# Kernel tuning notes

Hardware: AMD Instinct MI355X
Metric: run time of the kernel (lower is better)

## Reference

```python
import jax, jax.numpy as jnp
import numpy as np

NH = 16
NKV = 4
ROPE_BASE = 10000.0
ROPE_TSL = 1024
EPS = 1.1920928955078125e-07  # torch fp32 finfo eps (F.rms_norm default)


def _rms_norm(t):
    return t * jax.lax.rsqrt(jnp.mean(t * t, axis=-1, keepdims=True) + EPS)


def _rope_tables(T, hd):
    # Rotary with rd = hd (rope_dims=0 -> full-head rope). NTK rescale if T > tsl.
    rd = hd
    if T > ROPE_TSL:
        base = ROPE_BASE * (T / ROPE_TSL) ** (rd / (rd - 2))
    else:
        base = ROPE_BASE
    inv_freq = 1.0 / base ** (np.arange(0, rd, 2, dtype=np.float32) / rd)
    t = np.arange(T, dtype=np.float32)
    fr = np.outer(t, inv_freq)  # [T, hd//2]
    return jnp.asarray(np.cos(fr)), jnp.asarray(np.sin(fr))


def _apply_rope(x, cos, sin):
    # x: [B,T,H,D]; cos/sin: [T, D//2] broadcast over batch & heads
    h = x.shape[-1] // 2
    x1, x2 = x[..., :h], x[..., h:]
    c = cos[None, :, None, :]
    s = sin[None, :, None, :]
    return jnp.concatenate((x1 * c + x2 * s, -x1 * s + x2 * c), axis=-1)


def setup_inputs() -> dict:
    key = jax.random.key(0)
    k1, k2, k3, k4, k5 = jax.random.split(key, 5)
    B, T, dim = 2, 2048, 2048
    hd = dim // NH
    kd = NKV * hd
    std = 0.02
    return {
        "x": jax.random.normal(k1, (B, T, dim), dtype=jnp.float32),
        "Wq": jax.random.normal(k2, (dim, dim), dtype=jnp.float32) * std,
        "Wk": jax.random.normal(k3, (kd, dim), dtype=jnp.float32) * std,
        "Wv": jax.random.normal(k4, (kd, dim), dtype=jnp.float32) * std,
        "Wp": jax.random.normal(k5, (dim, dim), dtype=jnp.float32) * std,
        "q_gain": jnp.full((NH,), 1.5, dtype=jnp.float32),
    }


def reference(x, Wq, Wk, Wv, Wp, q_gain):
    B, T, d = x.shape
    hd = d // NH
    g = NH // NKV
    q = (x @ Wq.T).reshape(B, T, NH, hd)
    k = (x @ Wk.T).reshape(B, T, NKV, hd)
    v = (x @ Wv.T).reshape(B, T, NKV, hd)
    q = _rms_norm(q)
    k = _rms_norm(k)
    cos, sin = _rope_tables(T, hd)
    q = _apply_rope(q, cos, sin)
    k = _apply_rope(k, cos, sin)
    q = q * q_gain[None, None, :, None]
    # GQA causal SDPA: group queries per kv head
    qg = q.reshape(B, T, NKV, g, hd)
    scores = jnp.einsum("btkgd,bskd->bkgts", qg, k) / jnp.sqrt(jnp.asarray(hd, x.dtype))
    causal = jnp.tril(jnp.ones((T, T), dtype=bool))
    scores = jnp.where(causal[None, None, None, :, :], scores, jnp.asarray(-jnp.inf, scores.dtype))
    attn = jax.nn.softmax(scores, axis=-1)
    y = jnp.einsum("bkgts,bskd->btkgd", attn, v).reshape(B, T, d)
    return y @ Wp.T
```

## Files before the change

### kernel.cpp

```cpp
#include <hip/hip_runtime.h>
#include <math.h>

#define NH 16
#define NKV 4
#define HD 128
#define DIM 2048
#define GQ 4
#define EPS 1.1920928955078125e-07f

typedef unsigned short u16;
using bf16x8 = __attribute__((ext_vector_type(8))) short;
using f16x4  = __attribute__((ext_vector_type(4))) _Float16;
using f32x4  = __attribute__((ext_vector_type(4))) float;

__device__ inline float fast_exp2(float x) { return __builtin_amdgcn_exp2f(x); }

__device__ inline short f2bf(float f) {
    unsigned u = __builtin_bit_cast(unsigned, f);
    return (short)((u + 0x7FFFu + ((u >> 16) & 1u)) >> 16);
}
__device__ inline u16 f2h(float f) {
    _Float16 h = (_Float16)f;
    return __builtin_bit_cast(u16, h);
}

#define ASYNC_LOAD16(g, l)                                                        \
    __builtin_amdgcn_global_load_lds(                                             \
        (const __attribute__((address_space(1))) unsigned*)(g),                   \
        (__attribute__((address_space(3))) unsigned*)(l), 16, 0, 0)

__global__ __launch_bounds__(256) void cvt_bf16(const float* __restrict__ src,
                                                u16* __restrict__ dst, int n4) {
    int i = blockIdx.x * 256 + threadIdx.x;
    if (i < n4) {
        float4 f = ((const float4*)src)[i];
        ushort4 o;
        o.x = (u16)f2bf(f.x); o.y = (u16)f2bf(f.y);
        o.z = (u16)f2bf(f.z); o.w = (u16)f2bf(f.w);
        ((ushort4*)dst)[i] = o;
    }
}

__global__ __launch_bounds__(64) void rope_tab(float* __restrict__ ct,
                                               float* __restrict__ st,
                                               double base) {
    const int t = blockIdx.x;
    const int j = threadIdx.x;
    const float inv_freq = (float)pow(base, -(double)j / 64.0);
    const float fr = (float)t * inv_freq;
    ct[t * 64 + j] = cosf(fr);
    st[t * 64 + j] = sinf(fr);
}

#define BM 256
#define BN 256
#define BKT 64
#define NKT (DIM / BKT)

template <int EPI>
__global__ __launch_bounds__(512, 2) void gemm256(
    const u16* __restrict__ A, const u16* __restrict__ W,
    float* __restrict__ C, int N,
    u16* __restrict__ q16, u16* __restrict__ k16,
    u16* __restrict__ vt16,
    const float* __restrict__ ctab, const float* __restrict__ stab,
    const float* __restrict__ q_gain, int T) {
    __shared__ u16 As[2][BM * BKT];
    __shared__ u16 Bs[2][BN * BKT];

    const int tid  = threadIdx.x;
    const int wid  = tid >> 6;
    const int lane = tid & 63;
    const int l16  = lane & 15;
    const int quad = lane >> 4;
    const int wm   = wid >> 1;
    const int wn   = wid & 1;
    const int m0   = blockIdx.x * BM;
    const int n0   = blockIdx.y * BN;
    const int K    = DIM;

    const int srow = lane >> 3;
    const int scol = ((lane & 7) ^ srow) * 8;
    const u16* pa = A + (size_t)(m0 + srow) * K + scol;
    const u16* pw = W + (size_t)(n0 + srow) * K + scol;

    const int ca0 = ((quad)     ^ (l16 & 7)) * 8;
    const int ca1 = ((4 + quad) ^ (l16 & 7)) * 8;

    f32x4 acc[4][8];
#pragma unroll
    for (int i = 0; i < 4; i++)
#pragma unroll
        for (int j = 0; j < 8; j++) acc[i][j] = (f32x4){0.f, 0.f, 0.f, 0.f};

#pragma unroll
    for (int r = 0; r < 4; r++) {
        ASYNC_LOAD16(pa + (size_t)(r * 64 + wid * 8) * K, &As[0][(r * 64 + wid * 8) * BKT]);
        ASYNC_LOAD16(pw + (size_t)(r * 64 + wid * 8) * K, &Bs[0][(r * 64 + wid * 8) * BKT]);
    }
    __syncthreads();

#pragma unroll 1
    for (int kt = 0; kt < NKT; kt++) {
        const int cur = kt & 1;
        const u16* Ac = &As[cur][0];
        const u16* Bc = &Bs[cur][0];
        u16* An = &As[cur ^ 1][0];
        u16* Bn = &Bs[cur ^ 1][0];
        const bool pf = (kt + 1 < NKT);
        const size_t ko = (size_t)(kt + 1) * BKT;

        bf16x8 a0[4], a1[4];

        {
            bf16x8 bf[4];
#pragma unroll
            for (int mt = 0; mt < 4; mt++)
                a0[mt] = *(const bf16x8*)&Ac[(wm * 64 + mt * 16 + l16) * BKT + ca0];
#pragma unroll
            for (int nt = 0; nt < 4; nt++)
                bf[nt] = *(const bf16x8*)&Bc[(wn * 128 + nt * 16 + l16) * BKT + ca0];
            if (pf) {
                ASYNC_LOAD16(pa + (size_t)(0 * 64 + wid * 8) * K + ko, &An[(0 * 64 + wid * 8) * BKT]);
                ASYNC_LOAD16(pa + (size_t)(1 * 64 + wid * 8) * K + ko, &An[(1 * 64 + wid * 8) * BKT]);
            }
            __builtin_amdgcn_sched_barrier(0);
            __builtin_amdgcn_s_barrier();
            asm volatile("s_waitcnt lgkmcnt(0)" ::: "memory");
            __builtin_amdgcn_sched_barrier(0);
            __builtin_amdgcn_s_setprio(1);
#pragma unroll
            for (int mt = 0; mt < 4; mt++)
#pragma unroll
                for (int nt = 0; nt < 4; nt++)
                    acc[mt][nt] = __builtin_amdgcn_mfma_f32_16x16x32_bf16(
                        a0[mt], bf[nt], acc[mt][nt], 0, 0, 0);
            __builtin_amdgcn_s_setprio(0);
            __builtin_amdgcn_sched_barrier(0);
            __builtin_amdgcn_s_barrier();
        }

        {
            bf16x8 bf[4];
#pragma unroll
            for (int mt = 0; mt < 4; mt++)
                a1[mt] = *(const bf16x8*)&Ac[(wm * 64 + mt * 16 + l16) * BKT + ca1];
#pragma unroll
            for (int nt = 0; nt < 4; nt++)
                bf[nt] = *(const bf16x8*)&Bc[(wn * 128 + nt * 16 + l16) * BKT + ca1];
            if (pf) {
                ASYNC_LOAD16(pa + (size_t)(2 * 64 + wid * 8) * K + ko, &An[(2 * 64 + wid * 8) * BKT]);
                ASYNC_LOAD16(pa + (size_t)(3 * 64 + wid * 8) * K + ko, &An[(3 * 64 + wid * 8) * BKT]);
            }
            __builtin_amdgcn_sched_barrier(0);
            __builtin_amdgcn_s_barrier();
            asm volatile("s_waitcnt lgkmcnt(0)" ::: "memory");
            __builtin_amdgcn_sched_barrier(0);
            __builtin_amdgcn_s_setprio(1);
#pragma unroll
            for (int mt = 0; mt < 4; mt++)
#pragma unroll
                for (int nt = 0; nt < 4; nt++)
                    acc[mt][nt] = __builtin_amdgcn_mfma_f32_16x16x32_bf16(
                        a1[mt], bf[nt], acc[mt][nt], 0, 0, 0);
            __builtin_amdgcn_s_setprio(0);
            __builtin_amdgcn_sched_barrier(0);
            __builtin_amdgcn_s_barrier();
        }

        {
            bf16x8 bf[4];
#pragma unroll
            for (int nt = 0; nt < 4; nt++)
                bf[nt] = *(const bf16x8*)&Bc[(wn * 128 + (nt + 4) * 16 + l16) * BKT + ca0];
            if (pf) {
                ASYNC_LOAD16(pw + (size_t)(0 * 64 + wid * 8) * K + ko, &Bn[(0 * 64 + wid * 8) * BKT]);
                ASYNC_LOAD16(pw + (size_t)(1 * 64 + wid * 8) * K + ko, &Bn[(1 * 64 + wid * 8) * BKT]);
            }
            __builtin_amdgcn_sched_barrier(0);
            __builtin_amdgcn_s_barrier();
            asm volatile("s_waitcnt lgkmcnt(0)" ::: "memory");
            __builtin_amdgcn_sched_barrier(0);
            __builtin_amdgcn_s_setprio(1);
#pragma unroll
            for (int mt = 0; mt < 4; mt++)
#pragma unroll
                for (int nt = 0; nt < 4; nt++)
                    acc[mt][nt + 4] = __builtin_amdgcn_mfma_f32_16x16x32_bf16(
                        a0[mt], bf[nt], acc[mt][nt + 4], 0, 0, 0);
            __builtin_amdgcn_s_setprio(0);
            __builtin_amdgcn_sched_barrier(0);
            __builtin_amdgcn_s_barrier();
        }

        {
            bf16x8 bf[4];
#pragma unroll
            for (int nt = 0; nt < 4; nt++)
                bf[nt] = *(const bf16x8*)&Bc[(wn * 128 + (nt + 4) * 16 + l16) * BKT + ca1];
            if (pf) {
                ASYNC_LOAD16(pw + (size_t)(2 * 64 + wid * 8) * K + ko, &Bn[(2 * 64 + wid * 8) * BKT]);
                ASYNC_LOAD16(pw + (size_t)(3 * 64 + wid * 8) * K + ko, &Bn[(3 * 64 + wid * 8) * BKT]);
            }
            __builtin_amdgcn_sched_barrier(0);
            __builtin_amdgcn_s_barrier();
            asm volatile("s_waitcnt lgkmcnt(0)" ::: "memory");
            __builtin_amdgcn_sched_barrier(0);
            __builtin_amdgcn_s_setprio(1);
#pragma unroll
            for (int mt = 0; mt < 4; mt++)
#pragma unroll
                for (int nt = 0; nt < 4; nt++)
                    acc[mt][nt + 4] = __builtin_amdgcn_mfma_f32_16x16x32_bf16(
                        a1[mt], bf[nt], acc[mt][nt + 4], 0, 0, 0);
            __builtin_amdgcn_s_setprio(0);
        }

        __syncthreads();
    }

    if constexpr (EPI == 0) {
#pragma unroll
        for (int mt = 0; mt < 4; mt++)
#pragma unroll
            for (int nt = 0; nt < 8; nt++)
#pragma unroll
                for (int r = 0; r < 4; r++)
                    C[(size_t)(m0 + wm * 64 + mt * 16 + quad * 4 + r) * N +
                      n0 + wn * 128 + nt * 16 + l16] = acc[mt][nt][r];
    } else {
        const int nb = n0 + wn * 128;
        if (nb < 2560) {
            const bool isQ = (nb < 2048);
            const float gval =
                isQ ? (q_gain[nb >> 7] * 0.08838834764831843f * 1.4426950408889634f)
                    : 1.0f;
#pragma unroll
            for (int mt = 0; mt < 4; mt++) {
#pragma unroll
                for (int r = 0; r < 4; r++) {
                    float s = 0.f;
#pragma unroll
                    for (int nt = 0; nt < 8; nt++) {
                        float a = acc[mt][nt][r];
                        s = fmaf(a, a, s);
                    }
                    s += __shfl_xor(s, 1);
                    s += __shfl_xor(s, 2);
                    s += __shfl_xor(s, 4);
                    s += __shfl_xor(s, 8);
                    const float scale = rsqrtf(s * (1.0f / HD) + EPS) * gval;
                    const int m = m0 + wm * 64 + mt * 16 + quad * 4 + r;
                    const int t = m & (T - 1);
                    const float* ct = ctab + t * 64;
                    const float* st = stab + t * 64;
                    u16* dst = isQ ? (q16 + (size_t)m * 2048 + nb)
                                   : (k16 + (size_t)m * 512 + (nb - 2048));
#pragma unroll
                    for (int nt = 0; nt < 4; nt++) {
                        const int j = nt * 16 + l16;
                        const float c = ct[j], sn = st[j];
                        const float x1 = acc[mt][nt][r] * scale;
                        const float x2 = acc[mt][nt + 4][r] * scale;
                        dst[j]      = (u16)f2bf(x1 * c + x2 * sn);
                        dst[j + 64] = (u16)f2bf(x2 * c - x1 * sn);
                    }
                }
            }
        } else {
#pragma unroll
            for (int mt = 0; mt < 4; mt++) {
                const int mb = m0 + wm * 64 + mt * 16 + quad * 4;
                const int b = mb >> 11;
                const int t0 = mb & (T - 1);
#pragma unroll
                for (int nt = 0; nt < 8; nt++) {
                    const int dcol = nb - 2560 + nt * 16 + l16;
                    const int kvh = dcol >> 7;
                    const int d = dcol & (HD - 1);
                    ushort4 o;
                    o.x = f2h(acc[mt][nt][0]);
                    o.y = f2h(acc[mt][nt][1]);
                    o.z = f2h(acc[mt][nt][2]);
                    o.w = f2h(acc[mt][nt][3]);
                    *(ushort4*)(vt16 + ((size_t)((b * NKV + kvh) * HD + d)) * T + t0) = o;
                }
            }
        }
    }
}

#define QT 64
#define SK 64

__global__ __launch_bounds__(256) void flash4(const u16* __restrict__ q16,
                                              const u16* __restrict__ k16,
                                              const u16* __restrict__ vt16,
                                              u16* __restrict__ y16, int T) {
    __shared__ u16 Ks[2][SK * 128];
    __shared__ u16 Vt[2][HD * 64];

    const int tid = threadIdx.x;
    const int wave = tid >> 6;
    const int lane = tid & 63;
    const int l16 = lane & 15;
    const int quad = lane >> 4;

    const int bid = blockIdx.x;
    const int bh = bid & 31;
    const int pr = bid >> 5;
    const int h = bh & 15;
    const int b = bh >> 4;
    const int kv = h / GQ;

    const u16* kg = k16 + ((size_t)b * T * NKV + kv) * HD;
    const u16* vg = vt16 + (size_t)(b * NKV + kv) * HD * T;

    const int krow_in_seg = lane >> 4;
    const int kclog_base = lane & 15;
    const int vrow_in_seg = lane >> 3;
    const int vclog = (lane & 7) ^ (lane >> 3);

#pragma unroll 1
    for (int half = 0; half < 2; half++) {
        const int qt = half ? (T / QT - 1 - pr) : pr;
        const int q0 = qt * QT;
        const int qglob = q0 + wave * 16 + l16;
        const int nts = q0 / SK + 1;

        bf16x8 qf[4];
        {
            const u16* qp = q16 + ((size_t)(b * T + qglob) * NH + h) * HD;
#pragma unroll
            for (int kc = 0; kc < 4; kc++)
                qf[kc] = *(const bf16x8*)(qp + kc * 32 + quad * 8);
        }

        f32x4 of[8];
#pragma unroll
        for (int i = 0; i < 8; i++) of[i] = (f32x4){0.f, 0.f, 0.f, 0.f};
        float m_i = -1e30f, l_i = 0.0f;

        __syncthreads();
#pragma unroll
        for (int j = 0; j < 4; j++) {
            const int seg = wave * 4 + j;
            const int r = seg * 4 + krow_in_seg;
            const int clog = kclog_base ^ (r & 15);
            ASYNC_LOAD16(kg + (size_t)r * (NKV * HD) + clog * 8, &Ks[0][seg * 512]);
            const int d = seg * 8 + vrow_in_seg;
            ASYNC_LOAD16(vg + (size_t)d * T + vclog * 8, &Vt[0][seg * 512]);
        }

        for (int it = 0; it < nts; it++) {
            const int cur = it & 1;
            __syncthreads();

            if (it + 1 < nts) {
                const int s1 = (it + 1) * SK;
#pragma unroll
                for (int j = 0; j < 4; j++) {
                    const int seg = wave * 4 + j;
                    const int r = seg * 4 + krow_in_seg;
                    const int clog = kclog_base ^ (r & 15);
                    ASYNC_LOAD16(kg + (size_t)(s1 + r) * (NKV * HD) + clog * 8,
                                 &Ks[cur ^ 1][seg * 512]);
                    const int d = seg * 8 + vrow_in_seg;
                    ASYNC_LOAD16(vg + (size_t)d * T + s1 + vclog * 8,
                                 &Vt[cur ^ 1][seg * 512]);
                }
            }

            f32x4 sf[4];
#pragma unroll
            for (int st = 0; st < 4; st++) sf[st] = (f32x4){0.f, 0.f, 0.f, 0.f};
#pragma unroll
            for (int kc = 0; kc < 4; kc++)
#pragma unroll
                for (int st = 0; st < 4; st++) {
                    const int row = st * 16 + l16;
                    bf16x8 kf = *(const bf16x8*)
                        &Ks[cur][row * 128 + (((kc * 4 + quad) ^ l16) * 8)];
                    sf[st] = __builtin_amdgcn_mfma_f32_16x16x32_bf16(kf, qf[kc], sf[st], 0, 0, 0);
                }

            if (it == nts - 1) {
#pragma unroll
                for (int st = 0; st < 4; st++)
#pragma unroll
                    for (int r = 0; r < 4; r++)
                        if (q0 + st * 16 + quad * 4 + r > qglob) sf[st][r] = -1e30f;
            }

            float tm = -1e30f;
#pragma unroll
            for (int st = 0; st < 4; st++)
#pragma unroll
                for (int r = 0; r < 4; r++) tm = fmaxf(tm, sf[st][r]);
            tm = fmaxf(tm, __shfl_xor(tm, 16));
            tm = fmaxf(tm, __shfl_xor(tm, 32));

            const float mprev = m_i;
            const float mnew = fmaxf(mprev, tm);
            m_i = mnew;
            const float alpha = fast_exp2(mprev - mnew);

            f16x4 pf[4];
            float ls = 0.0f;
#pragma unroll
            for (int st = 0; st < 4; st++)
#pragma unroll
                for (int r = 0; r < 4; r++) {
                    float e = fast_exp2(sf[st][r] - mnew);
                    ls += e;
                    pf[st][r] = (_Float16)e;
                }
            ls += __shfl_xor(ls, 16);
            ls += __shfl_xor(ls, 32);
            l_i = alpha * l_i + ls;

            if (__ballot(mnew > mprev)) {
#pragma unroll
                for (int dt = 0; dt < 8; dt++)
#pragma unroll
                    for (int r = 0; r < 4; r++) of[dt][r] *= alpha;
            }

#pragma unroll
            for (int st = 0; st < 4; st++) {
                const int clog = st * 2 + (quad >> 1);
#pragma unroll
                for (int dt = 0; dt < 8; dt++) {
                    const int d = dt * 16 + l16;
                    const int phys = clog ^ (l16 & 7);
                    f16x4 va = *(const f16x4*)
                        &Vt[cur][d * 64 + phys * 8 + (quad & 1) * 4];
                    of[dt] = __builtin_amdgcn_mfma_f32_16x16x16f16(va, pf[st], of[dt], 0, 0, 0);
                }
            }
        }

        const float inv = 1.0f / l_i;
        u16* yp = y16 + ((size_t)(b * T + qglob) * NH + h) * HD + quad * 4;
#pragma unroll
        for (int dt = 0; dt < 8; dt++) {
            ushort4 o;
            o.x = (u16)f2bf(of[dt][0] * inv);
            o.y = (u16)f2bf(of[dt][1] * inv);
            o.z = (u16)f2bf(of[dt][2] * inv);
            o.w = (u16)f2bf(of[dt][3] * inv);
            *(ushort4*)(yp + dt * 16) = o;
        }
    }
}

extern "C" void kernel_launch(void* const* d_in, const int* in_sizes, int n_in,
                              void* d_out, int out_size, void* d_ws, size_t ws_size,
                              hipStream_t stream) {
    const float* x      = (const float*)d_in[0];
    const float* Wq     = (const float*)d_in[1];
    const float* Wk     = (const float*)d_in[2];
    const float* Wv     = (const float*)d_in[3];
    const float* Wp     = (const float*)d_in[4];
    const float* q_gain = (const float*)d_in[5];
    float* out = (float*)d_out;

    const int B = 2;
    const int BT = in_sizes[0] / DIM;
    const int T = BT / B;
    const int KD = NKV * HD;

    u16* x16   = (u16*)d_ws;
    u16* wqkv  = x16 + (size_t)BT * DIM;
    u16* wp16  = wqkv + (size_t)3072 * DIM;
    u16* q16   = wp16 + (size_t)DIM * DIM;
    u16* k16   = q16 + (size_t)BT * DIM;
    u16* vt16  = k16 + (size_t)BT * KD;
    float* ctab = (float*)(vt16 + (size_t)BT * KD);
    float* stab = ctab + (size_t)T * 64;
    u16* y16   = x16;

    double base = 10000.0;
    if (T > 1024) base = 10000.0 * pow((double)T / 1024.0, 128.0 / 126.0);

    const int nx4  = BT * DIM / 4;
    const int nwq4 = DIM * DIM / 4;
    const int nwk4 = KD * DIM / 4;

    cvt_bf16<<<(nx4 + 255) / 256, 256, 0, stream>>>(x, x16, nx4);
    cvt_bf16<<<(nwq4 + 255) / 256, 256, 0, stream>>>(Wq, wqkv, nwq4);
    cvt_bf16<<<(nwk4 + 255) / 256, 256, 0, stream>>>(Wk, wqkv + (size_t)2048 * DIM, nwk4);
    cvt_bf16<<<(nwk4 + 255) / 256, 256, 0, stream>>>(Wv, wqkv + (size_t)2560 * DIM, nwk4);
    cvt_bf16<<<(nwq4 + 255) / 256, 256, 0, stream>>>(Wp, wp16, nwq4);
    rope_tab<<<T, 64, 0, stream>>>(ctab, stab, base);

    gemm256<1><<<dim3(BT / BM, 3072 / BN), 512, 0, stream>>>(
        x16, wqkv, nullptr, 0, q16, k16, vt16, ctab, stab, q_gain, T);

    flash4<<<32 * (T / QT / 2), 256, 0, stream>>>(q16, k16, vt16, y16, T);

    gemm256<0><<<dim3(BT / BM, DIM / BN), 512, 0, stream>>>(
        y16, wp16, out, DIM, nullptr, nullptr, nullptr, nullptr, nullptr, nullptr, T);
}
```

Before: 318.5 us.

## Replace full syncthreads with split vmcnt waits in GEMM prefetch pipeline

Reorders the GEMM's async global-to-LDS prefetches so that all A rows are issued first and the B halves are interleaved (rows 0/2 then 1/3). The per-iteration __syncthreads is replaced with partial s_waitcnt vmcnt waits plus raw s_barriers, so only the needed half of the next tile must have landed before its consumption phase. Prefetch is made unconditional by wrapping the k offset (extra redundant loads on the last iteration, drained by a final vmcnt(0)). It relies on exact vmcnt counting being correct; miscounted waits would race. The output-projection launch grid is rewritten as DIM/128/2, which appears equivalent to DIM/BN if BN is 256.

```diff
diff --git a/kernel.cpp b/kernel.cpp
--- a/kernel.cpp
+++ b/kernel.cpp
@@ -28,6 +28,10 @@
     __builtin_amdgcn_global_load_lds(                                             \
         (const __attribute__((address_space(1))) unsigned*)(g),                   \
         (__attribute__((address_space(3))) unsigned*)(l), 16, 0, 0)
+
+#define SCHED_FENCE() __builtin_amdgcn_sched_barrier(0)
+#define WAIT_LGKM0()  asm volatile("s_waitcnt lgkmcnt(0)" ::: "memory")
+#define WAIT_VM(N)    asm volatile("s_waitcnt vmcnt(" #N ")" ::: "memory")
 
 __global__ __launch_bounds__(256) void cvt_bf16(const float* __restrict__ src,
                                                 u16* __restrict__ dst, int n4) {
@@ -94,11 +98,16 @@
         for (int j = 0; j < 8; j++) acc[i][j] = (f32x4){0.f, 0.f, 0.f, 0.f};
 
 #pragma unroll
-    for (int r = 0; r < 4; r++) {
+    for (int r = 0; r < 4; r++)
         ASYNC_LOAD16(pa + (size_t)(r * 64 + wid * 8) * K, &As[0][(r * 64 + wid * 8) * BKT]);
-        ASYNC_LOAD16(pw + (size_t)(r * 64 + wid * 8) * K, &Bs[0][(r * 64 + wid * 8) * BKT]);
-    }
-    __syncthreads();
+    ASYNC_LOAD16(pw + (size_t)(0 * 64 + wid * 8) * K, &Bs[0][(0 * 64 + wid * 8) * BKT]);
+    ASYNC_LOAD16(pw + (size_t)(2 * 64 + wid * 8) * K, &Bs[0][(2 * 64 + wid * 8) * BKT]);
+    ASYNC_LOAD16(pw + (size_t)(1 * 64 + wid * 8) * K, &Bs[0][(1 * 64 + wid * 8) * BKT]);
+    ASYNC_LOAD16(pw + (size_t)(3 * 64 + wid * 8) * K, &Bs[0][(3 * 64 + wid * 8) * BKT]);
+    WAIT_VM(2);
+    SCHED_FENCE();
+    __builtin_amdgcn_s_barrier();
+    SCHED_FENCE();
 
 #pragma unroll 1
     for (int kt = 0; kt < NKT; kt++) {
@@ -107,8 +116,7 @@
         const u16* Bc = &Bs[cur][0];
         u16* An = &As[cur ^ 1][0];
         u16* Bn = &Bs[cur ^ 1][0];
-        const bool pf = (kt + 1 < NKT);
-        const size_t ko = (size_t)(kt + 1) * BKT;
+        const size_t ko = (size_t)((kt + 1) & (NKT - 1)) * BKT;
 
         bf16x8 a0[4], a1[4];
 
@@ -120,14 +128,14 @@
 #pragma unroll
             for (int nt = 0; nt < 4; nt++)
                 bf[nt] = *(const bf16x8*)&Bc[(wn * 128 + nt * 16 + l16) * BKT + ca0];
-            if (pf) {
-                ASYNC_LOAD16(pa + (size_t)(0 * 64 + wid * 8) * K + ko, &An[(0 * 64 + wid * 8) * BKT]);
-                ASYNC_LOAD16(pa + (size_t)(1 * 64 + wid * 8) * K + ko, &An[(1 * 64 + wid * 8) * BKT]);
-            }
-            __builtin_amdgcn_sched_barrier(0);
-            __builtin_amdgcn_s_barrier();
-            asm volatile("s_waitcnt lgkmcnt(0)" ::: "memory");
-            __builtin_amdgcn_sched_barrier(0);
+#pragma unroll
+            for (int r = 0; r < 4; r++)
+                ASYNC_LOAD16(pa + (size_t)(r * 64 + wid * 8) * K + ko,
+                             &An[(r * 64 + wid * 8) * BKT]);
+            SCHED_FENCE();
+            __builtin_amdgcn_s_barrier();
+            WAIT_LGKM0();
+            SCHED_FENCE();
             __builtin_amdgcn_s_setprio(1);
 #pragma unroll
             for (int mt = 0; mt < 4; mt++)
@@ -136,7 +144,7 @@
                     acc[mt][nt] = __builtin_amdgcn_mfma_f32_16x16x32_bf16(
                         a0[mt], bf[nt], acc[mt][nt], 0, 0, 0);
             __builtin_amdgcn_s_setprio(0);
-            __builtin_amdgcn_sched_barrier(0);
+            SCHED_FENCE();
             __builtin_amdgcn_s_barrier();
         }
 
@@ -148,14 +156,14 @@
 #pragma unroll
             for (int nt = 0; nt < 4; nt++)
                 bf[nt] = *(const bf16x8*)&Bc[(wn * 128 + nt * 16 + l16) * BKT + ca1];
-            if (pf) {
-                ASYNC_LOAD16(pa + (size_t)(2 * 64 + wid * 8) * K + ko, &An[(2 * 64 + wid * 8) * BKT]);
-                ASYNC_LOAD16(pa + (size_t)(3 * 64 + wid * 8) * K + ko, &An[(3 * 64 + wid * 8) * BKT]);
-            }
-            __builtin_amdgcn_sched_barrier(0);
-            __builtin_amdgcn_s_barrier();
-            asm volatile("s_waitcnt lgkmcnt(0)" ::: "memory");
-            __builtin_amdgcn_sched_barrier(0);
+            ASYNC_LOAD16(pw + (size_t)(0 * 64 + wid * 8) * K + ko,
+                         &Bn[(0 * 64 + wid * 8) * BKT]);
+            ASYNC_LOAD16(pw + (size_t)(2 * 64 + wid * 8) * K + ko,
+                         &Bn[(2 * 64 + wid * 8) * BKT]);
+            SCHED_FENCE();
+            __builtin_amdgcn_s_barrier();
+            WAIT_LGKM0();
+            SCHED_FENCE();
             __builtin_amdgcn_s_setprio(1);
 #pragma unroll
             for (int mt = 0; mt < 4; mt++)
@@ -164,8 +172,10 @@
                     acc[mt][nt] = __builtin_amdgcn_mfma_f32_16x16x32_bf16(
                         a1[mt], bf[nt], acc[mt][nt], 0, 0, 0);
             __builtin_amdgcn_s_setprio(0);
-            __builtin_amdgcn_sched_barrier(0);
-            __builtin_amdgcn_s_barrier();
+            WAIT_VM(6);
+            SCHED_FENCE();
+            __builtin_amdgcn_s_barrier();
+            SCHED_FENCE();
         }
 
         {
@@ -173,14 +183,14 @@
 #pragma unroll
             for (int nt = 0; nt < 4; nt++)
                 bf[nt] = *(const bf16x8*)&Bc[(wn * 128 + (nt + 4) * 16 + l16) * BKT + ca0];
-            if (pf) {
-                ASYNC_LOAD16(pw + (size_t)(0 * 64 + wid * 8) * K + ko, &Bn[(0 * 64 + wid * 8) * BKT]);
-                ASYNC_LOAD16(pw + (size_t)(1 * 64 + wid * 8) * K + ko, &Bn[(1 * 64 + wid * 8) * BKT]);
-            }
-            __builtin_amdgcn_sched_barrier(0);
-            __builtin_amdgcn_s_barrier();
-            asm volatile("s_waitcnt lgkmcnt(0)" ::: "memory");
-            __builtin_amdgcn_sched_barrier(0);
+            ASYNC_LOAD16(pw + (size_t)(1 * 64 + wid * 8) * K + ko,
+                         &Bn[(1 * 64 + wid * 8) * BKT]);
+            ASYNC_LOAD16(pw + (size_t)(3 * 64 + wid * 8) * K + ko,
+                         &Bn[(3 * 64 + wid * 8) * BKT]);
+            SCHED_FENCE();
+            __builtin_amdgcn_s_barrier();
+            WAIT_LGKM0();
+            SCHED_FENCE();
             __builtin_amdgcn_s_setprio(1);
 #pragma unroll
             for (int mt = 0; mt < 4; mt++)
@@ -189,7 +199,7 @@
                     acc[mt][nt + 4] = __builtin_amdgcn_mfma_f32_16x16x32_bf16(
                         a0[mt], bf[nt], acc[mt][nt + 4], 0, 0, 0);
             __builtin_amdgcn_s_setprio(0);
-            __builtin_amdgcn_sched_barrier(0);
+            SCHED_FENCE();
             __builtin_amdgcn_s_barrier();
         }
 
@@ -198,14 +208,10 @@
 #pragma unroll
             for (int nt = 0; nt < 4; nt++)
                 bf[nt] = *(const bf16x8*)&Bc[(wn * 128 + (nt + 4) * 16 + l16) * BKT + ca1];
-            if (pf) {
-                ASYNC_LOAD16(pw + (size_t)(2 * 64 + wid * 8) * K + ko, &Bn[(2 * 64 + wid * 8) * BKT]);
-                ASYNC_LOAD16(pw + (size_t)(3 * 64 + wid * 8) * K + ko, &Bn[(3 * 64 + wid * 8) * BKT]);
-            }
-            __builtin_amdgcn_sched_barrier(0);
-            __builtin_amdgcn_s_barrier();
-            asm volatile("s_waitcnt lgkmcnt(0)" ::: "memory");
-            __builtin_amdgcn_sched_barrier(0);
+            SCHED_FENCE();
+            __builtin_amdgcn_s_barrier();
+            WAIT_LGKM0();
+            SCHED_FENCE();
             __builtin_amdgcn_s_setprio(1);
 #pragma unroll
             for (int mt = 0; mt < 4; mt++)
@@ -214,10 +220,13 @@
                     acc[mt][nt + 4] = __builtin_amdgcn_mfma_f32_16x16x32_bf16(
                         a1[mt], bf[nt], acc[mt][nt + 4], 0, 0, 0);
             __builtin_amdgcn_s_setprio(0);
-        }
-
-        __syncthreads();
+            WAIT_VM(2);
+            SCHED_FENCE();
+            __builtin_amdgcn_s_barrier();
+            SCHED_FENCE();
+        }
     }
+    WAIT_VM(0);
 
     if constexpr (EPI == 0) {
 #pragma unroll
@@ -499,6 +508,6 @@
 
     flash4<<<32 * (T / QT / 2), 256, 0, stream>>>(q16, k16, vt16, y16, T);
 
-    gemm256<0><<<dim3(BT / BM, DIM / BN), 512, 0, stream>>>(
+    gemm256<0><<<dim3(BT / BM, DIM / 128 / 2), 512, 0, stream>>>(
         y16, wp16, out, DIM, nullptr, nullptr, nullptr, nullptr, nullptr, nullptr, T);
 }
```

Measured after the change: 324.8 us. Within noise of the previous version (+2.0%).
